# Performance work log

Measured on AMD Instinct MI355X. Metric: run time of the kernel, lower is better.

The kernel has to match this reference:

```python
import jax, jax.numpy as jnp
import numpy as np
from jax import lax

B, T, IN, H, DIM = 128, 1024, 64, 128, 64


def setup_inputs() -> dict:
    key = jax.random.key(0)
    ks = jax.random.split(key, 14)
    s = 0.05
    return {
        "x": jax.random.normal(ks[0], (B, T, IN), jnp.float32),
        "is_init": jax.random.randint(ks[1], (B, T, 1), 0, 2).astype(bool),
        "hx": jax.random.normal(ks[2], (B, H), jnp.float32),
        # MLP: Linear(IN,128) + ELU, Linear(128,128) + ELU
        "W1": jax.random.normal(ks[3], (128, IN), jnp.float32) * s,
        "b1": jnp.zeros((128,), jnp.float32),
        "W2": jax.random.normal(ks[4], (128, 128), jnp.float32) * s,
        "b2": jnp.zeros((128,), jnp.float32),
        # GRU params (torch layout: [3H, in] with gate order r,z,n)
        "W_ih": jax.random.normal(ks[5], (3 * H, 128), jnp.float32) * s,
        "b_ih": jnp.zeros((3 * H,), jnp.float32),
        "W_hh": jax.random.normal(ks[6], (3 * H, H), jnp.float32) * s,
        "b_hh": jnp.zeros((3 * H,), jnp.float32),
        # output head Linear(128, DIM)
        "W_out": jax.random.normal(ks[7], (DIM, 128), jnp.float32) * s,
        "b_out": jnp.zeros((DIM,), jnp.float32),
    }


def _gru_with_reset(xg, init_mask, h0, W_hh, b_hh):
    # xg: [T,B,3H] precomputed input-side gates; init_mask: [T,B,1] float
    def step(h, inp):
        xg_t, m_t = inp
        h = h * (1.0 - m_t)                       # reset hidden where is_init
        hg = h @ W_hh.T + b_hh                    # [B,3H]
        xr, xz, xn = jnp.split(xg_t, 3, axis=-1)
        hr, hz, hn = jnp.split(hg, 3, axis=-1)
        r = jax.nn.sigmoid(xr + hr)
        z = jax.nn.sigmoid(xz + hz)
        n = jnp.tanh(xn + r * hn)
        h_new = (1.0 - z) * n + z * h
        return h_new, h_new

    hT, ys = lax.scan(step, h0, (xg, init_mask))
    return ys, hT


def reference(x, is_init, hx, W1, b1, W2, b2, W_ih, b_ih, W_hh, b_hh, W_out, b_out):
    # MLP (ELU activations)
    h = jax.nn.elu(x @ W1.T + b1)
    h = jax.nn.elu(h @ W2.T + b2)                 # [B,T,128]
    # precompute input-side gate projections for all timesteps (one big GEMM)
    xg = h @ W_ih.T + b_ih                        # [B,T,3H]
    xg_t = jnp.transpose(xg, (1, 0, 2))           # [T,B,3H]
    m_t = jnp.transpose(is_init.astype(x.dtype), (1, 0, 2))  # [T,B,1]
    ys, hT = _gru_with_reset(xg_t, m_t, hx, W_hh, b_hh)
    y = jnp.transpose(ys, (1, 0, 2))              # [B,T,H]
    out = y @ W_out.T + b_out                     # [B,T,DIM]
    return out, hT
```

## Files before the change

kernel.cpp:

```cpp
#include <hip/hip_runtime.h>


#define T_SZ 1024

typedef __attribute__((ext_vector_type(8))) short short8;
typedef __attribute__((ext_vector_type(4))) float f32x4;
typedef unsigned long long u64;
typedef unsigned int uint32;

__device__ __forceinline__ unsigned short f2b(float f){
  return __builtin_bit_cast(unsigned short, (__bf16)f);
}
__device__ __forceinline__ float b2f(unsigned int hs){
  unsigned int u = hs << 16;
  return __builtin_bit_cast(float, u);
}
__device__ __forceinline__ float rcp_f(float x){ return __builtin_amdgcn_rcpf(x); }
__device__ __forceinline__ float elu(float v){ return v > 0.f ? v : __expf(v) - 1.f; }
__device__ __forceinline__ float sigm(float x){ return rcp_f(1.f + __expf(-x)); }
__device__ __forceinline__ float tanh_fast(float x){
  x = fminf(fmaxf(x, -15.f), 15.f);
  float e = __expf(-2.f * x);
  return (1.f - e) * rcp_f(1.f + e);
}
#define MFMA16(a,b,c) __builtin_amdgcn_mfma_f32_16x16x32_bf16(a, b, c, 0, 0, 0)


__global__ __launch_bounds__(512) void wprep(
    const float* __restrict__ Whh, const float* __restrict__ W1,
    const float* __restrict__ W2,  const float* __restrict__ Wih,
    uint4* __restrict__ wtab)
{
  int rec = blockIdx.x*512 + threadIdx.x;
  if(rec >= 15360) return;
  const float* p;
  if(rec < 6144){
    int q = rec & 3, n_ = (rec >> 2) & 127, ks = (rec >> 9) & 3, gt = rec >> 11;
    p = Whh + (size_t)(n_ + 128*gt)*128 + ks*32 + q*8;
  } else if(rec < 7168){
    int r = rec - 6144;
    int q = r & 3, n_ = (r >> 2) & 127, ks = r >> 9;
    p = W1 + (size_t)n_*64 + ks*32 + q*8;
  } else if(rec < 9216){
    int r = rec - 7168;
    int q = r & 3, n_ = (r >> 2) & 127, ks = r >> 9;
    p = W2 + (size_t)n_*128 + ks*32 + q*8;
  } else {
    int r = rec - 9216;
    int q = r & 3, n_ = (r >> 2) & 127, ks = (r >> 9) & 3, gt = r >> 11;
    p = Wih + (size_t)(n_ + 128*gt)*128 + ks*32 + q*8;
  }
  uint4 o;
  o.x = (uint32)f2b(p[0]) | ((uint32)f2b(p[1]) << 16);
  o.y = (uint32)f2b(p[2]) | ((uint32)f2b(p[3]) << 16);
  o.z = (uint32)f2b(p[4]) | ((uint32)f2b(p[5]) << 16);
  o.w = (uint32)f2b(p[6]) | ((uint32)f2b(p[7]) << 16);
  wtab[rec] = o;
}

__global__ __launch_bounds__(512) void seg_build(const int* __restrict__ ii, uint32* C){
  __shared__ uint32 lh[1024];
  __shared__ uint32 lbase[1024];
  __shared__ uint32 ssum[512];
  __shared__ uint32 sbase;
  uint32* segs = C + 4096;
  const int tid = threadIdx.x;
  const int wv = tid >> 6, lane = tid & 63;
  const int b = blockIdx.x*8 + wv;

  for(int i = tid; i < 1024; i += 512) lh[i] = 0u;
  __syncthreads();

  u64 bal[16], mb[16];
  #pragma unroll
  for(int c=0;c<16;c++){
    int t = c*64 + lane;
    int m = ii[b*T_SZ + t];
    mb[c]  = __ballot(m != 0);
    bal[c] = __ballot((m != 0) || (t == 0));
  }
  int fsA[16]; int nx = T_SZ;
  #pragma unroll
  for(int c=15;c>=0;c--){ fsA[c]=nx; if(bal[c]) nx = c*64 + __builtin_ctzll(bal[c]); }

  int lenA[16], tA[16], rkA[16];
  #pragma unroll
  for(int c=0;c<16;c++){
    lenA[c] = 0;
    if((bal[c] >> lane) & 1ull){
      int t = c*64 + lane;
      u64 hi = (lane < 63) ? (bal[c] >> (lane+1)) : 0ull;
      int nxt = hi ? (t + 1 + __builtin_ctzll(hi)) : fsA[c];
      int len = nxt - t;
      int rst = (int)((mb[c] >> lane) & 1ull);
      len -= rst; t += rst;
      if(len > 0){
        lenA[c] = len; tA[c] = t;
        rkA[c] = (int)atomicAdd(&lh[1024 - len], 1u);
      }
    }
  }
  __syncthreads();

  uint32 c0 = lh[2*tid], c1 = lh[2*tid+1];
  ssum[tid] = c0 + c1;
  __syncthreads();
  #pragma unroll
  for(int off=1; off<512; off<<=1){
    uint32 v = (tid >= off) ? ssum[tid-off] : 0u;
    __syncthreads();
    ssum[tid] += v;
    __syncthreads();
  }
  uint32 excl = tid ? ssum[tid-1] : 0u;
  lbase[2*tid]   = excl;
  lbase[2*tid+1] = excl + c0;
  uint32 total = ssum[511];
  uint32 padded = (total + 15u) & ~15u;
  if(tid == 0){
    sbase = atomicAdd(&C[2], padded);
    atomicAdd(&C[1], padded >> 4);
  }
  __syncthreads();
  const uint32 base = sbase;

  #pragma unroll
  for(int c=0;c<16;c++){
    if(lenA[c] > 0){
      uint32 slot = base + lbase[1024 - lenA[c]] + (uint32)rkA[c];
      segs[slot] = ((uint32)b << 21) | ((uint32)tA[c] << 11) | (uint32)lenA[c];
    }
  }
  for(uint32 i = total + tid; i < padded; i += 512) segs[base + i] = 0u;
}

__global__ __launch_bounds__(512) void mlp2(
    const float* __restrict__ x,
    const uint4* __restrict__ wtab,
    const float* __restrict__ b1, const float* __restrict__ b2,
    unsigned short* __restrict__ h2)
{
  __shared__ __align__(16) char smem[35840];
  unsigned short* xs  = (unsigned short*)smem;
  unsigned short* h1l = (unsigned short*)(smem + 18432);
  const int tid = threadIdx.x;
  const int wv = tid >> 6, l = tid & 63, quad = l >> 4, col = l & 15;
  const int n = 16*wv + col;

  short8 w1f[2], w2f[4];
  #pragma unroll
  for(int ks=0; ks<2; ks++)
    w1f[ks] = __builtin_bit_cast(short8, wtab[6144 + (ks*128 + n)*4 + quad]);
  #pragma unroll
  for(int ks=0; ks<4; ks++)
    w2f[ks] = __builtin_bit_cast(short8, wtab[7168 + (ks*128 + n)*4 + quad]);
  const float b1v = b1[n], b2v = b2[n];

  const int srow = tid >> 5, sk = tid & 31;

  for(int tile = blockIdx.x; tile < 2048; tile += gridDim.x){
    const int g = tile & 7, t0 = (tile >> 3) * 4;
    {
      const float* src = x + (size_t)(16*g + srow)*(T_SZ*64) + (size_t)t0*64;
      #pragma unroll
      for(int j=0; j<2; j++){
        int s = sk + 32*j;
        float4 v = ((const float4*)src)[s];
        int tt = s >> 4, k = (s & 15) * 4;
        unsigned short* dst = xs + (tt*16 + srow)*72 + k;
        dst[0]=f2b(v.x); dst[1]=f2b(v.y); dst[2]=f2b(v.z); dst[3]=f2b(v.w);
      }
    }
    __syncthreads();
    #pragma unroll
    for(int tt=0; tt<4; tt++){
      f32x4 acc = {b1v, b1v, b1v, b1v};
      #pragma unroll
      for(int ks=0; ks<2; ks++){
        short8 a = *(const short8*)&xs[(tt*16 + col)*72 + ks*32 + quad*8];
        acc = MFMA16(a, w1f[ks], acc);
      }
      #pragma unroll
      for(int r=0; r<4; r++)
        h1l[(tt*16 + quad*4 + r)*136 + n] = f2b(elu(acc[r]));
    }
    __syncthreads();
    #pragma unroll
    for(int tt=0; tt<4; tt++){
      f32x4 acc = {b2v, b2v, b2v, b2v};
      #pragma unroll
      for(int ks=0; ks<4; ks++){
        short8 a = *(const short8*)&h1l[(tt*16 + col)*136 + ks*32 + quad*8];
        acc = MFMA16(a, w2f[ks], acc);
      }
      const int t = t0 + tt;
      #pragma unroll
      for(int r=0; r<4; r++){
        int row = quad*4 + r;
        h2[((size_t)(t*8 + g)*16 + row)*128 + n] = f2b(elu(acc[r]));
      }
    }
  }
}

__global__ __launch_bounds__(512) void xgproj(
    const unsigned short* h2, const int* __restrict__ ii,
    const uint4* __restrict__ wtab,
    const float* __restrict__ bih, const float* __restrict__ bhh,
    unsigned short* __restrict__ xg, unsigned short* ys,
    float* __restrict__ hT)
{
  __shared__ __align__(16) unsigned short h2l[4*16*136];
  __shared__ int iil[64];
  const int tid = threadIdx.x;
  const int wv = tid >> 6, l = tid & 63, quad = l >> 4, col = l & 15;
  const int n = 16*wv + col;

  short8 wif[3][4];
  #pragma unroll
  for(int gt=0; gt<3; gt++){
    #pragma unroll
    for(int ks=0; ks<4; ks++)
      wif[gt][ks] = __builtin_bit_cast(short8, wtab[9216 + ((gt*4 + ks)*128 + n)*4 + quad]);
  }
  float bihv[3], bhhv[3];
  #pragma unroll
  for(int gt=0; gt<3; gt++){ bihv[gt] = bih[n + 128*gt]; bhhv[gt] = bhh[n + 128*gt]; }

  for(int tile = blockIdx.x; tile < 2048; tile += gridDim.x){
    const int g = tile & 7, t0 = (tile >> 3) * 4;
    {
      const int w = tid >> 3, j = tid & 7;
      const int tt = w >> 4, row = w & 15;
      const unsigned short* src = h2 + ((size_t)((t0 + tt)*8 + g)*16 + row)*128 + j*16;
      unsigned short* dst = &h2l[(tt*16 + row)*136 + j*16];
      #pragma unroll
      for(int i2=0; i2<4; i2++)
        *(u64*)(dst + i2*4) = *(const u64*)(src + i2*4);
    }
    if(tid < 64) iil[tid] = ii[(16*g + (tid & 15))*T_SZ + t0 + (tid >> 4)];
    __syncthreads();

    uint32 xgo[4];
    #pragma unroll
    for(int r=0; r<4; r++)
      xgo[r] = (((uint32)(16*g + quad*4 + r) << 10) + (uint32)t0) * 384u + (uint32)n;
    #pragma unroll
    for(int tt=0; tt<4; tt++){
      f32x4 a0 = {bihv[0], bihv[0], bihv[0], bihv[0]};
      f32x4 a1 = {bihv[1], bihv[1], bihv[1], bihv[1]};
      f32x4 a2 = {bihv[2], bihv[2], bihv[2], bihv[2]};
      #pragma unroll
      for(int ks=0; ks<4; ks++){
        short8 a = *(const short8*)&h2l[(tt*16 + col)*136 + ks*32 + quad*8];
        a0 = MFMA16(a, wif[0][ks], a0);
        a1 = MFMA16(a, wif[1][ks], a1);
        a2 = MFMA16(a, wif[2][ks], a2);
      }
      const int t = t0 + tt;
      #pragma unroll
      for(int r=0; r<4; r++){
        int row = quad*4 + r;
        if(iil[tt*16 + row] != 0){
          float rr = sigm(a0[r] + bhhv[0]);
          float zz = sigm(a1[r] + bhhv[1]);
          float nn = tanh_fast(a2[r] + rr*bhhv[2]);
          float h1 = (1.f - zz)*nn;
          ys[((size_t)(t*8 + g)*16 + row)*128 + n] = f2b(h1);
          if(t == T_SZ-1)
            hT[(16*g + row)*128 + n] = h1;
        } else {
          unsigned short* p = xg + xgo[r] + (uint32)(tt*384);
          p[0]   = f2b(a0[r]);
          p[128] = f2b(a1[r]);
          p[256] = f2b(a2[r]);
        }
      }
    }
    __syncthreads();
  }
}

__global__ __launch_bounds__(512) void gru_seg_scan(
    const unsigned short* __restrict__ xg,
    const float* __restrict__ hx,
    const uint4* __restrict__ wbf, const float* __restrict__ bhh,
    const uint32* __restrict__ C,
    unsigned short* __restrict__ ys, float* __restrict__ hT)
{
  __shared__ unsigned short hl[2][16*136];
  __shared__ unsigned short xbuf[2][16*388];
  __shared__ int srb[16], srt[16], srlen[16];
  const uint32 ntile = C[1];
  const uint32 tile = blockIdx.x;
  if(tile >= ntile) return;

  const int tid = threadIdx.x;
  const int wv = tid >> 6, l = tid & 63, quad = l >> 4, col = l & 15;
  const int nidx = 16*wv + col;
  const int frow = tid >> 5, fk = tid & 31;
  const uint32* segs = C + 4096;

  short8 whf[3][4];
  float bhv[3];
  #pragma unroll
  for(int gt=0; gt<3; gt++){
    bhv[gt] = bhh[nidx + 128*gt];
    #pragma unroll
    for(int ks=0; ks<4; ks++){
      uint4 w = wbf[((gt*4 + ks)*128 + nidx)*4 + quad];
      whf[gt][ks] = __builtin_bit_cast(short8, w);
    }
  }

  if(tid < 16){
    uint32 w = segs[16*tile + (uint32)tid];
    srb[tid] = (int)(w >> 21);
    srt[tid] = (int)((w >> 11) & 1023u);
    srlen[tid] = (int)(w & 2047u);
  }
  __syncthreads();
  const int maxlen = srlen[0];
  const int fb = srb[frow], ft = srt[frow], fl = srlen[frow];

  float hreg[4];
  #pragma unroll
  for(int r=0; r<4; r++){
    int row = quad*4 + r;
    int b = srb[row], t0 = srt[row];
    float h0 = 0.f;
    if(srlen[row] > 0){
      h0 = (t0 == 0) ? hx[b*128 + nidx]
                     : b2f(ys[((size_t)((t0-1)*8 + (b>>4))*16 + (b&15))*128 + nidx]);
    }
    hreg[r] = h0;
    hl[0][row*136 + nidx] = f2b(h0);
  }
  {
    const unsigned short* src = xg + ((size_t)fb*T_SZ + ft)*384;
    unsigned short* xb = &xbuf[0][frow*388];
    #pragma unroll
    for(int i2=0; i2<3; i2++)
      *(u64*)(xb + i2*128 + fk*4) = *(const u64*)(src + i2*128 + fk*4);
  }

  int cur = 0;
  for(int i=0; i<maxlen; i++){
    __syncthreads();
    short8 af[4];
    #pragma unroll
    for(int ks=0; ks<4; ks++)
      af[ks] = *(const short8*)&hl[cur][col*136 + ks*32 + quad*8];
    f32x4 ar = {bhv[0], bhv[0], bhv[0], bhv[0]};
    f32x4 az = {bhv[1], bhv[1], bhv[1], bhv[1]};
    f32x4 an = {bhv[2], bhv[2], bhv[2], bhv[2]};
    #pragma unroll
    for(int ks=0; ks<4; ks++){
      ar = MFMA16(af[ks], whf[0][ks], ar);
      az = MFMA16(af[ks], whf[1][ks], az);
      an = MFMA16(af[ks], whf[2][ks], an);
    }
    u64 p0, p1, p2;
    {
      int tc = (i+1 < fl) ? i+1 : (fl > 0 ? fl-1 : 0);
      const unsigned short* src = xg + ((size_t)fb*T_SZ + (ft + tc))*384;
      p0 = *(const u64*)(src +       fk*4);
      p1 = *(const u64*)(src + 128 + fk*4);
      p2 = *(const u64*)(src + 256 + fk*4);
    }
    if(i >= 1 && i <= fl){
      int t = ft + i - 1;
      u64 hv = *(const u64*)&hl[cur][frow*136 + fk*4];
      *(u64*)(ys + ((size_t)(t*8 + (fb>>4))*16 + (fb&15))*128 + fk*4) = hv;
      if(i == fl && ft + fl == T_SZ){
        #pragma unroll
        for(int j=0; j<4; j++)
          hT[fb*128 + fk*4 + j] = b2f(hl[cur][frow*136 + fk*4 + j]);
      }
    }
    const unsigned short* xb = &xbuf[cur][0];
    #pragma unroll
    for(int r=0; r<4; r++){
      int row = quad*4 + r;
      float xrv = b2f(xb[row*388 +       nidx]);
      float xzv = b2f(xb[row*388 + 128 + nidx]);
      float xnv = b2f(xb[row*388 + 256 + nidx]);
      float rr = sigm(xrv + ar[r]);
      float zz = sigm(xzv + az[r]);
      float nn = tanh_fast(xnv + rr*an[r]);
      float hnew = (1.f - zz)*nn + zz*hreg[r];
      hreg[r] = hnew;
      hl[cur^1][row*136 + nidx] = f2b(hnew);
    }
    {
      unsigned short* xb2 = &xbuf[cur^1][frow*388];
      *(u64*)(xb2 +       fk*4) = p0;
      *(u64*)(xb2 + 128 + fk*4) = p1;
      *(u64*)(xb2 + 256 + fk*4) = p2;
    }
    cur ^= 1;
  }
  __syncthreads();
  if(maxlen >= 1 && fl == maxlen){
    int t = ft + maxlen - 1;
    u64 hv = *(const u64*)&hl[cur][frow*136 + fk*4];
    *(u64*)(ys + ((size_t)(t*8 + (fb>>4))*16 + (fb&15))*128 + fk*4) = hv;
    if(ft + fl == T_SZ){
      #pragma unroll
      for(int j=0; j<4; j++)
        hT[fb*128 + fk*4 + j] = b2f(hl[cur][frow*136 + fk*4 + j]);
    }
  }
}

__global__ __launch_bounds__(256) void out_gemm(
    const unsigned short* __restrict__ ys,
    const float* __restrict__ Wout, const float* __restrict__ bout,
    float* __restrict__ outp)
{
  const int tid = threadIdx.x;
  const int wv = tid >> 6, l = tid & 63, quad = l >> 4, col = l & 15;
  const int n = 16*wv + col;
  short8 wof[4];
  #pragma unroll
  for(int ks=0; ks<4; ks++){
    const float* p = Wout + n*128 + ks*32 + quad*8;
    const float4* q = (const float4*)p;
    float4 u0 = q[0], u1 = q[1];
    short8 v;
    v[0]=(short)f2b(u0.x); v[1]=(short)f2b(u0.y); v[2]=(short)f2b(u0.z); v[3]=(short)f2b(u0.w);
    v[4]=(short)f2b(u1.x); v[5]=(short)f2b(u1.y); v[6]=(short)f2b(u1.z); v[7]=(short)f2b(u1.w);
    wof[ks] = v;
  }
  const float bov = bout[n];
  for(int tile = blockIdx.x; tile < 8192; tile += gridDim.x){
    const int t = tile >> 3, g = tile & 7;
    const unsigned short* yt = ys + (size_t)tile * 16 * 128;
    f32x4 acc = {bov, bov, bov, bov};
    #pragma unroll
    for(int ks=0; ks<4; ks++){
      short8 a = *(const short8*)&yt[col*128 + ks*32 + quad*8];
      acc = MFMA16(a, wof[ks], acc);
    }
    #pragma unroll
    for(int r=0; r<4; r++)
      outp[(size_t)(16*g + quad*4 + r)*(T_SZ*64) + (size_t)t*64 + n] = acc[r];
  }
}

extern "C" void kernel_launch(void* const* d_in, const int* in_sizes, int n_in,
                              void* d_out, int out_size, void* d_ws, size_t ws_size,
                              hipStream_t stream)
{
  const float* x    = (const float*)d_in[0];
  const int*   ii   = (const int*)  d_in[1];
  const float* hx   = (const float*)d_in[2];
  const float* W1   = (const float*)d_in[3];
  const float* b1   = (const float*)d_in[4];
  const float* W2   = (const float*)d_in[5];
  const float* b2   = (const float*)d_in[6];
  const float* Wih  = (const float*)d_in[7];
  const float* bih  = (const float*)d_in[8];
  const float* Whh  = (const float*)d_in[9];
  const float* bhh  = (const float*)d_in[10];
  const float* Wout = (const float*)d_in[11];
  const float* bout = (const float*)d_in[12];

  float* outp = (float*)d_out;
  float* hT   = outp + (size_t)128 * T_SZ * 64;
  uint32* C   = (uint32*)d_out;
  uint4* wtab = (uint4*)((char*)d_out + (1u<<20));

  unsigned short* xg = (unsigned short*)d_ws;
  unsigned short* ys = (unsigned short*)((char*)d_ws + 100663296ull);

  hipMemsetAsync(C, 0, 64, stream);
  wprep      <<<dim3(30),   dim3(512),  0, stream>>>(Whh, W1, W2, Wih, wtab);
  seg_build  <<<dim3(16),   dim3(512),  0, stream>>>(ii, C);
  mlp2       <<<dim3(2048), dim3(512),  0, stream>>>(x, wtab, b1, b2, ys);
  xgproj     <<<dim3(2048), dim3(512),  0, stream>>>(ys, ii, wtab, bih, bhh, xg, ys, hT);
  gru_seg_scan<<<dim3(4160),dim3(512),  0, stream>>>(xg, hx, wtab, bhh, C, ys, hT);
  out_gemm   <<<dim3(2048), dim3(256),  0, stream>>>(ys, Wout, bout, outp);
}
```

Baseline: 225.4 us.

## Make GRU segment scan persistent with zig-zag tile assignment, halve MLP grids

```diff
diff --git a/kernel.cpp b/kernel.cpp
--- a/kernel.cpp
+++ b/kernel.cpp
@@ -200,6 +200,7 @@
         h2[((size_t)(t*8 + g)*16 + row)*128 + n] = f2b(elu(acc[r]));
       }
     }
+    __syncthreads();
   }
 }
 
@@ -292,8 +293,6 @@
   __shared__ unsigned short xbuf[2][16*388];
   __shared__ int srb[16], srt[16], srlen[16];
   const uint32 ntile = C[1];
-  const uint32 tile = blockIdx.x;
-  if(tile >= ntile) return;
 
   const int tid = threadIdx.x;
   const int wv = tid >> 6, l = tid & 63, quad = l >> 4, col = l & 15;
@@ -313,102 +312,120 @@
     }
   }
 
-  if(tid < 16){
-    uint32 w = segs[16*tile + (uint32)tid];
-    srb[tid] = (int)(w >> 21);
-    srt[tid] = (int)((w >> 11) & 1023u);
-    srlen[tid] = (int)(w & 2047u);
-  }
-  __syncthreads();
-  const int maxlen = srlen[0];
-  const int fb = srb[frow], ft = srt[frow], fl = srlen[frow];
-
-  float hreg[4];
-  #pragma unroll
-  for(int r=0; r<4; r++){
-    int row = quad*4 + r;
-    int b = srb[row], t0 = srt[row];
-    float h0 = 0.f;
-    if(srlen[row] > 0){
-      h0 = (t0 == 0) ? hx[b*128 + nidx]
-                     : b2f(ys[((size_t)((t0-1)*8 + (b>>4))*16 + (b&15))*128 + nidx]);
-    }
-    hreg[r] = h0;
-    hl[0][row*136 + nidx] = f2b(h0);
-  }
-  {
-    const unsigned short* src = xg + ((size_t)fb*T_SZ + ft)*384;
-    unsigned short* xb = &xbuf[0][frow*388];
-    #pragma unroll
-    for(int i2=0; i2<3; i2++)
-      *(u64*)(xb + i2*128 + fk*4) = *(const u64*)(src + i2*128 + fk*4);
-  }
-
-  int cur = 0;
-  for(int i=0; i<maxlen; i++){
-    __syncthreads();
-    short8 af[4];
-    #pragma unroll
-    for(int ks=0; ks<4; ks++)
-      af[ks] = *(const short8*)&hl[cur][col*136 + ks*32 + quad*8];
-    f32x4 ar = {bhv[0], bhv[0], bhv[0], bhv[0]};
-    f32x4 az = {bhv[1], bhv[1], bhv[1], bhv[1]};
-    f32x4 an = {bhv[2], bhv[2], bhv[2], bhv[2]};
-    #pragma unroll
-    for(int ks=0; ks<4; ks++){
-      ar = MFMA16(af[ks], whf[0][ks], ar);
-      az = MFMA16(af[ks], whf[1][ks], az);
-      an = MFMA16(af[ks], whf[2][ks], an);
-    }
-    u64 p0, p1, p2;
+  for(int p = 0; p < 4; p++){
+    __syncthreads();
+    const uint32 tile = (uint32)((p >> 1) * 2080)
+                      + ((p & 1) ? (uint32)(2079 - (int)blockIdx.x) : blockIdx.x);
+    if(tile >= ntile) continue;
+
+    if(tid < 16){
+      uint32 w = segs[16*tile + (uint32)tid];
+      srb[tid] = (int)(w >> 21);
+      srt[tid] = (int)((w >> 11) & 1023u);
+      srlen[tid] = (int)(w & 2047u);
+    }
+    __syncthreads();
+    const int maxlen = srlen[0];
+    const int fb = srb[frow], ft = srt[frow], fl = srlen[frow];
+
     {
-      int tc = (i+1 < fl) ? i+1 : (fl > 0 ? fl-1 : 0);
-      const unsigned short* src = xg + ((size_t)fb*T_SZ + (ft + tc))*384;
-      p0 = *(const u64*)(src +       fk*4);
-      p1 = *(const u64*)(src + 128 + fk*4);
-      p2 = *(const u64*)(src + 256 + fk*4);
-    }
-    if(i >= 1 && i <= fl){
-      int t = ft + i - 1;
+      if(fl > 0){
+        if(ft == 0){
+          float4 hv = *(const float4*)(hx + fb*128 + fk*4);
+          unsigned short* d = &hl[0][frow*136 + fk*4];
+          d[0]=f2b(hv.x); d[1]=f2b(hv.y); d[2]=f2b(hv.z); d[3]=f2b(hv.w);
+        } else {
+          u64 hv = *(const u64*)(ys + ((size_t)((ft-1)*8 + (fb>>4))*16 + (fb&15))*128 + fk*4);
+          *(u64*)&hl[0][frow*136 + fk*4] = hv;
+        }
+      } else {
+        *(u64*)&hl[0][frow*136 + fk*4] = 0ull;
+      }
+    }
+    {
+      const unsigned short* src = xg + ((size_t)fb*T_SZ + ft)*384;
+      unsigned short* xb = &xbuf[0][frow*388];
+      #pragma unroll
+      for(int i2=0; i2<3; i2++)
+        *(u64*)(xb + i2*128 + fk*4) = *(const u64*)(src + i2*128 + fk*4);
+    }
+    __syncthreads();
+
+    float hreg[4];
+    #pragma unroll
+    for(int r=0; r<4; r++){
+      int row = quad*4 + r;
+      hreg[r] = (srlen[row] > 0 && srt[row] == 0)
+                  ? hx[srb[row]*128 + nidx]
+                  : b2f(hl[0][row*136 + nidx]);
+    }
+
+    int cur = 0;
+    for(int i=0; i<maxlen; i++){
+      __syncthreads();
+      short8 af[4];
+      #pragma unroll
+      for(int ks=0; ks<4; ks++)
+        af[ks] = *(const short8*)&hl[cur][col*136 + ks*32 + quad*8];
+      f32x4 ar = {bhv[0], bhv[0], bhv[0], bhv[0]};
+      f32x4 az = {bhv[1], bhv[1], bhv[1], bhv[1]};
+      f32x4 an = {bhv[2], bhv[2], bhv[2], bhv[2]};
+      #pragma unroll
+      for(int ks=0; ks<4; ks++){
+        ar = MFMA16(af[ks], whf[0][ks], ar);
+        az = MFMA16(af[ks], whf[1][ks], az);
+        an = MFMA16(af[ks], whf[2][ks], an);
+      }
+      u64 p0, p1, p2;
+      {
+        int tc = (i+1 < fl) ? i+1 : (fl > 0 ? fl-1 : 0);
+        const unsigned short* src = xg + ((size_t)fb*T_SZ + (ft + tc))*384;
+        p0 = *(const u64*)(src +       fk*4);
+        p1 = *(const u64*)(src + 128 + fk*4);
+        p2 = *(const u64*)(src + 256 + fk*4);
+      }
+      if(i >= 1 && i <= fl){
+        int t = ft + i - 1;
+        u64 hv = *(const u64*)&hl[cur][frow*136 + fk*4];
+        *(u64*)(ys + ((size_t)(t*8 + (fb>>4))*16 + (fb&15))*128 + fk*4) = hv;
+        if(i == fl && ft + fl == T_SZ){
+          #pragma unroll
+          for(int j=0; j<4; j++)
+            hT[fb*128 + fk*4 + j] = b2f(hl[cur][frow*136 + fk*4 + j]);
+        }
+      }
+      const unsigned short* xb = &xbuf[cur][0];
+      #pragma unroll
+      for(int r=0; r<4; r++){
+        int row = quad*4 + r;
+        float xrv = b2f(xb[row*388 +       nidx]);
+        float xzv = b2f(xb[row*388 + 128 + nidx]);
+        float xnv = b2f(xb[row*388 + 256 + nidx]);
+        float rr = sigm(xrv + ar[r]);
+        float zz = sigm(xzv + az[r]);
+        float nn = tanh_fast(xnv + rr*an[r]);
+        float hnew = (1.f - zz)*nn + zz*hreg[r];
+        hreg[r] = hnew;
+        hl[cur^1][row*136 + nidx] = f2b(hnew);
+      }
+      {
+        unsigned short* xb2 = &xbuf[cur^1][frow*388];
+        *(u64*)(xb2 +       fk*4) = p0;
+        *(u64*)(xb2 + 128 + fk*4) = p1;
+        *(u64*)(xb2 + 256 + fk*4) = p2;
+      }
+      cur ^= 1;
+    }
+    __syncthreads();
+    if(maxlen >= 1 && fl == maxlen){
+      int t = ft + maxlen - 1;
       u64 hv = *(const u64*)&hl[cur][frow*136 + fk*4];
       *(u64*)(ys + ((size_t)(t*8 + (fb>>4))*16 + (fb&15))*128 + fk*4) = hv;
-      if(i == fl && ft + fl == T_SZ){
+      if(ft + fl == T_SZ){
         #pragma unroll
         for(int j=0; j<4; j++)
           hT[fb*128 + fk*4 + j] = b2f(hl[cur][frow*136 + fk*4 + j]);
       }
-    }
-    const unsigned short* xb = &xbuf[cur][0];
-    #pragma unroll
-    for(int r=0; r<4; r++){
-      int row = quad*4 + r;
-      float xrv = b2f(xb[row*388 +       nidx]);
-      float xzv = b2f(xb[row*388 + 128 + nidx]);
-      float xnv = b2f(xb[row*388 + 256 + nidx]);
-      float rr = sigm(xrv + ar[r]);
-      float zz = sigm(xzv + az[r]);
-      float nn = tanh_fast(xnv + rr*an[r]);
-      float hnew = (1.f - zz)*nn + zz*hreg[r];
-      hreg[r] = hnew;
-      hl[cur^1][row*136 + nidx] = f2b(hnew);
-    }
-    {
-      unsigned short* xb2 = &xbuf[cur^1][frow*388];
-      *(u64*)(xb2 +       fk*4) = p0;
-      *(u64*)(xb2 + 128 + fk*4) = p1;
-      *(u64*)(xb2 + 256 + fk*4) = p2;
-    }
-    cur ^= 1;
-  }
-  __syncthreads();
-  if(maxlen >= 1 && fl == maxlen){
-    int t = ft + maxlen - 1;
-    u64 hv = *(const u64*)&hl[cur][frow*136 + fk*4];
-    *(u64*)(ys + ((size_t)(t*8 + (fb>>4))*16 + (fb&15))*128 + fk*4) = hv;
-    if(ft + fl == T_SZ){
-      #pragma unroll
-      for(int j=0; j<4; j++)
-        hT[fb*128 + fk*4 + j] = b2f(hl[cur][frow*136 + fk*4 + j]);
     }
   }
 }
@@ -477,8 +494,8 @@
   hipMemsetAsync(C, 0, 64, stream);
   wprep      <<<dim3(30),   dim3(512),  0, stream>>>(Whh, W1, W2, Wih, wtab);
   seg_build  <<<dim3(16),   dim3(512),  0, stream>>>(ii, C);
-  mlp2       <<<dim3(2048), dim3(512),  0, stream>>>(x, wtab, b1, b2, ys);
-  xgproj     <<<dim3(2048), dim3(512),  0, stream>>>(ys, ii, wtab, bih, bhh, xg, ys, hT);
-  gru_seg_scan<<<dim3(4160),dim3(512),  0, stream>>>(xg, hx, wtab, bhh, C, ys, hT);
+  mlp2       <<<dim3(1024), dim3(512),  0, stream>>>(x, wtab, b1, b2, ys);
+  xgproj     <<<dim3(1024), dim3(512),  0, stream>>>(ys, ii, wtab, bih, bhh, xg, ys, hT);
+  gru_seg_scan<<<dim3(1040),dim3(512),  0, stream>>>(xg, hx, wtab, bhh, C, ys, hT);
   out_gemm   <<<dim3(2048), dim3(256),  0, stream>>>(ys, Wout, bout, outp);
 }
```

After: 231.2 us. +2.6%, slower.
